# Performance work log

Measured on AMD Instinct MI355X. Metric: run time of the kernel, lower is better.

## Reference

```python
import jax, jax.numpy as jnp
import numpy as np

N = 500_000
IN_FEAT = 128
HIDDEN = 128
OUT_FEAT = 128
CODE_DIM = 32
NUM_CODES = 256


def _linear_params(key, fan_in, fan_out):
    kw, kb = jax.random.split(key)
    bound = 1.0 / np.sqrt(fan_in)
    W = jax.random.uniform(kw, (fan_out, fan_in), jnp.float32, -bound, bound)
    b = jax.random.uniform(kb, (fan_out,), jnp.float32, -bound, bound)
    return W, b


def setup_inputs() -> dict:
    key = jax.random.key(0)
    ks = jax.random.split(key, 6)
    x = jax.random.normal(ks[0], (N, IN_FEAT), jnp.float32)
    W_down, b_down = _linear_params(ks[1], IN_FEAT, HIDDEN)
    W_pin, b_pin = _linear_params(ks[2], HIDDEN, CODE_DIM)      # VQ project_in 128->32
    codebook = jax.random.normal(ks[3], (NUM_CODES, CODE_DIM), jnp.float32)
    W_pout, b_pout = _linear_params(ks[4], CODE_DIM, HIDDEN)    # VQ project_out 32->128
    W_up, b_up = _linear_params(ks[5], HIDDEN, OUT_FEAT)
    return {"x": x, "W_down": W_down, "b_down": b_down,
            "W_pin": W_pin, "b_pin": b_pin, "codebook": codebook,
            "W_pout": W_pout, "b_pout": b_pout,
            "W_up": W_up, "b_up": b_up}


def reference(x, W_down, b_down, W_pin, b_pin, codebook, W_pout, b_pout, W_up, b_up):
    # down: Linear(128 -> 128)
    h = x @ W_down.T + b_down                                   # [N, 128]
    # VQ project_in: Linear(128 -> 32)
    z = h @ W_pin.T + b_pin                                     # [N, 32]
    # squared euclidean distance to codebook, argmin assignment
    d2 = (jnp.sum(z * z, axis=-1, keepdims=True)
          - 2.0 * (z @ codebook.T)
          + jnp.sum(codebook * codebook, axis=-1))              # [N, 256]
    indices = jnp.argmin(d2, axis=-1)                           # [N] int
    q = codebook[indices]                                       # gather [N, 32]
    # straight-through estimator
    q_ste = z + jax.lax.stop_gradient(q - z)
    # VQ project_out: Linear(32 -> 128)
    v = q_ste @ W_pout.T + b_pout                               # [N, 128]
    # up: Linear(128 -> 128), then clamp
    y = jnp.clip(v @ W_up.T + b_up, -1.0, 1.0)                  # [N, 128]
    # commitment_weight = 0 -> commit loss is exactly zero
    commit_loss = jnp.zeros((), x.dtype)
    return y, indices, commit_loss
```

## Files before the change

### kernel.cpp

```cpp
#include <hip/hip_runtime.h>


#define CODE_D 32
#define NUM_C  256


__global__ void vq_prep1(const float* __restrict__ Wd, const float* __restrict__ bd,
                         const float* __restrict__ Wp, const float* __restrict__ bp,
                         const float* __restrict__ cb,
                         float* __restrict__ Wc, float* __restrict__ bc,
                         float* __restrict__ cbias) {
    const int t = threadIdx.x;
    const int b = blockIdx.x;
    if (b < 16) {
        const int e = b * 256 + t;
        const int j = e >> 7, k = e & 127;
        double s0 = 0.0, s1 = 0.0;
#pragma unroll 8
        for (int m = 0; m < 128; m += 2) {
            s0 += (double)Wp[j * 128 + m]     * (double)Wd[(m) * 128 + k];
            s1 += (double)Wp[j * 128 + m + 1] * (double)Wd[(m + 1) * 128 + k];
        }
        Wc[e] = (float)(s0 + s1);
    } else if (b == 16) {
        if (t < 32) {
            double s = (double)bp[t];
            for (int m = 0; m < 128; ++m) s += (double)Wp[t * 128 + m] * (double)bd[m];
            bc[t] = (float)s;
        }
    } else {
        float s = 0.f;
#pragma unroll
        for (int d = 0; d < CODE_D; ++d) { float v = cb[t * CODE_D + d]; s += v * v; }
        cbias[t] = -0.5f * s;
    }
}

__global__ void vq_prep2(const float* __restrict__ cb, const float* __restrict__ Wpo,
                         const float* __restrict__ bpo, const float* __restrict__ Wu,
                         const float* __restrict__ bu, float* __restrict__ ytab) {
    __shared__ float v[128];
    const int c = blockIdx.x;
    const int t = threadIdx.x;
    float s = bpo[t];
    for (int d = 0; d < CODE_D; ++d) s += cb[c * CODE_D + d] * Wpo[t * CODE_D + d];
    v[t] = s;
    __syncthreads();
    float o = bu[t];
    for (int m = 0; m < 128; ++m) o += v[m] * Wu[t * 128 + m];
    o = fminf(fmaxf(o, -1.0f), 1.0f);
    ytab[c * 128 + t] = o;
}


__global__ __launch_bounds__(256, 6) void vq_main(
    const float* __restrict__ x,
    const float* __restrict__ Wc,
    const float* __restrict__ bc,
    const float* __restrict__ cb,
    const float* __restrict__ cbias,
    const float* __restrict__ ytab,
    float* __restrict__ y,
    float* __restrict__ idx_out,
    float* __restrict__ loss_out,
    int N) {
    __shared__ int sidx[256];

    const int t = threadIdx.x;
    const int row0 = blockIdx.x * 256;
    const int myrow = row0 + t;
    const int rd = myrow < N ? myrow : (N - 1);

    float z[CODE_D];
#pragma unroll
    for (int j = 0; j < CODE_D; ++j) z[j] = bc[j];

    const float* __restrict__ xr = x + (size_t)rd * 128;
#pragma unroll
    for (int q = 0; q < 32; ++q) {
        const float4 xv = *reinterpret_cast<const float4*>(xr + q * 4);
        const int kb = q * 4;
#pragma unroll
        for (int j = 0; j < CODE_D; ++j) {
            const float* w = Wc + j * 128 + kb;
            z[j] += w[0] * xv.x + w[1] * xv.y + w[2] * xv.z + w[3] * xv.w;
        }
    }

    float best = -3.0e38f;
    int besti = 0;
#pragma unroll 4
    for (int c = 0; c < NUM_C; ++c) {
        const float* crow = cb + c * CODE_D;
        float s0 = 0.f, s1 = 0.f, s2 = 0.f, s3 = 0.f;
#pragma unroll
        for (int d = 0; d < CODE_D; d += 4) {
            s0 += crow[d + 0] * z[d + 0];
            s1 += crow[d + 1] * z[d + 1];
            s2 += crow[d + 2] * z[d + 2];
            s3 += crow[d + 3] * z[d + 3];
        }
        const float s = ((s0 + s1) + (s2 + s3)) + cbias[c];
        if (s > best) { best = s; besti = c; }
    }

    sidx[t] = besti;
    if (myrow < N) idx_out[myrow] = (float)besti;
    __syncthreads();

    const int rsub = t >> 5;
    const int c4 = t & 31;
#pragma unroll
    for (int i = 0; i < 32; ++i) {
        const int r = i * 8 + rsub;
        const int grow = row0 + r;
        if (grow < N) {
            const int ci = sidx[r];
            const float4 v = *reinterpret_cast<const float4*>(ytab + ci * 128 + c4 * 4);
            *reinterpret_cast<float4*>(y + (size_t)grow * 128 + c4 * 4) = v;
        }
    }

    if (blockIdx.x == 0 && t == 0) loss_out[0] = 0.0f;
}


extern "C" void kernel_launch(void* const* d_in, const int* in_sizes, int n_in,
                              void* d_out, int out_size, void* d_ws, size_t ws_size,
                              hipStream_t stream) {
    const float* x   = (const float*)d_in[0];
    const float* Wd  = (const float*)d_in[1];
    const float* bd  = (const float*)d_in[2];
    const float* Wp  = (const float*)d_in[3];
    const float* bp  = (const float*)d_in[4];
    const float* cb  = (const float*)d_in[5];
    const float* Wpo = (const float*)d_in[6];
    const float* bpo = (const float*)d_in[7];
    const float* Wu  = (const float*)d_in[8];
    const float* bu  = (const float*)d_in[9];

    const int N = in_sizes[0] / 128;

    float* ws    = (float*)d_ws;
    float* Wc    = ws;
    float* bc    = ws + 4096;
    float* cbias = ws + 4128;
    float* ytab  = ws + 4384;

    float* y    = (float*)d_out;
    float* idxf = y + (size_t)N * 128;
    float* loss = idxf + N;

    vq_prep1<<<18, 256, 0, stream>>>(Wd, bd, Wp, bp, cb, Wc, bc, cbias);
    vq_prep2<<<NUM_C, 128, 0, stream>>>(cb, Wpo, bpo, Wu, bu, ytab);

    const int blocks = (N + 255) / 256;
    vq_main<<<blocks, 256, 0, stream>>>(x, Wc, bc, cb, cbias, ytab, y, idxf, loss, N);
}
```

Before: 962.5 us.

## Stage x tiles and codebook through LDS in VQ main kernel

Loads of x now go through shared memory in 16-column chunks using coalesced float4 loads across threads, instead of each thread reading its own 512-byte row directly from global memory. The codebook is copied into LDS in two 128-code passes, and the code biases are copied too, so the argmin loop reads shared memory instead of global/scalar memory. This targets uncoalesced x access and repeated global codebook reads, but adds many __syncthreads barriers and about 21 KB of LDS per block, which may reduce occupancy. Codebook reads from LDS are uniform broadcasts, where they were previously scalar loads from global memory.

Result: faster. 876.0 us (-9.0%).

```diff
diff --git a/kernel.cpp b/kernel.cpp
--- a/kernel.cpp
+++ b/kernel.cpp
@@ -3,6 +3,8 @@
 
 #define CODE_D 32
 #define NUM_C  256
+#define KCH    16
+#define LSTR   20
 
 
 __global__ void vq_prep1(const float* __restrict__ Wd, const float* __restrict__ bd,
@@ -64,44 +66,73 @@
     float* __restrict__ idx_out,
     float* __restrict__ loss_out,
     int N) {
+    __shared__ float lds[256 * LSTR];
+    __shared__ float scb[NUM_C];
     __shared__ int sidx[256];
 
     const int t = threadIdx.x;
     const int row0 = blockIdx.x * 256;
     const int myrow = row0 + t;
-    const int rd = myrow < N ? myrow : (N - 1);
 
     float z[CODE_D];
 #pragma unroll
     for (int j = 0; j < CODE_D; ++j) z[j] = bc[j];
 
-    const float* __restrict__ xr = x + (size_t)rd * 128;
+    scb[t] = cbias[t];
+
+    const int rr = t >> 2;
+    const int qq = t & 3;
+    for (int kc = 0; kc < 128; kc += KCH) {
 #pragma unroll
-    for (int q = 0; q < 32; ++q) {
-        const float4 xv = *reinterpret_cast<const float4*>(xr + q * 4);
-        const int kb = q * 4;
+        for (int i = 0; i < 4; ++i) {
+            const int r = i * 64 + rr;
+            const int grow = row0 + r;
+            float4 v = make_float4(0.f, 0.f, 0.f, 0.f);
+            if (grow < N)
+                v = *reinterpret_cast<const float4*>(x + (size_t)grow * 128 + kc + qq * 4);
+            *reinterpret_cast<float4*>(&lds[r * LSTR + qq * 4]) = v;
+        }
+        __syncthreads();
 #pragma unroll
-        for (int j = 0; j < CODE_D; ++j) {
-            const float* w = Wc + j * 128 + kb;
-            z[j] += w[0] * xv.x + w[1] * xv.y + w[2] * xv.z + w[3] * xv.w;
+        for (int q = 0; q < KCH / 4; ++q) {
+            const float4 xv = *reinterpret_cast<const float4*>(&lds[t * LSTR + q * 4]);
+            const int kb = kc + q * 4;
+#pragma unroll
+            for (int j = 0; j < CODE_D; ++j) {
+                const float* w = Wc + j * 128 + kb;
+                z[j] += w[0] * xv.x + w[1] * xv.y + w[2] * xv.z + w[3] * xv.w;
+            }
         }
+        __syncthreads();
     }
 
     float best = -3.0e38f;
     int besti = 0;
+#pragma unroll
+    for (int pass = 0; pass < 2; ++pass) {
+        const float4* cb4 = reinterpret_cast<const float4*>(cb) + pass * 1024;
+#pragma unroll
+        for (int i = 0; i < 4; ++i)
+            reinterpret_cast<float4*>(lds)[i * 256 + t] = cb4[i * 256 + t];
+        __syncthreads();
+
+        const int cb0 = pass << 7;
 #pragma unroll 4
-    for (int c = 0; c < NUM_C; ++c) {
-        const float* crow = cb + c * CODE_D;
-        float s0 = 0.f, s1 = 0.f, s2 = 0.f, s3 = 0.f;
+        for (int i = 0; i < 128; ++i) {
+            const int c = cb0 + i;
+            const float* crow = &lds[i * CODE_D];
+            float s0 = 0.f, s1 = 0.f, s2 = 0.f, s3 = 0.f;
 #pragma unroll
-        for (int d = 0; d < CODE_D; d += 4) {
-            s0 += crow[d + 0] * z[d + 0];
-            s1 += crow[d + 1] * z[d + 1];
-            s2 += crow[d + 2] * z[d + 2];
-            s3 += crow[d + 3] * z[d + 3];
+            for (int d = 0; d < CODE_D; d += 4) {
+                s0 += crow[d + 0] * z[d + 0];
+                s1 += crow[d + 1] * z[d + 1];
+                s2 += crow[d + 2] * z[d + 2];
+                s3 += crow[d + 3] * z[d + 3];
+            }
+            const float s = ((s0 + s1) + (s2 + s3)) + scb[c];
+            if (s > best) { best = s; besti = c; }
         }
-        const float s = ((s0 + s1) + (s2 + s3)) + cbias[c];
-        if (s > best) { best = s; besti = c; }
+        __syncthreads();
     }
 
     sidx[t] = besti;
```
